# Performance work log

Measured on AMD Instinct MI355X. Metric: run time of the kernel, lower is better.

The kernel has to match this reference:

```python
import jax, jax.numpy as jnp
import numpy as np

H = 1024        # hidden_size
I = 2048        # intermediate_size
E = 8           # num_experts
K = 2           # num_experts_per_tok
AUX_COEF = 0.01
Z_COEF = 0.001


def setup_inputs() -> dict:
    key = jax.random.key(0)
    ks = jax.random.split(key, 8)
    s = 0.02
    return {
        "hidden_states": jax.random.normal(ks[0], (1, 2048, H), dtype=jnp.float32),
        "router_w": jax.random.normal(ks[1], (H, E), dtype=jnp.float32) * s,
        "eg": jax.random.normal(ks[2], (E, H, I), dtype=jnp.float32) * s,  # gate_proj per expert
        "eu": jax.random.normal(ks[3], (E, H, I), dtype=jnp.float32) * s,  # up_proj per expert
        "ed": jax.random.normal(ks[4], (E, I, H), dtype=jnp.float32) * s,  # down_proj per expert
        "sg": jax.random.normal(ks[5], (H, I), dtype=jnp.float32) * s,     # shared expert gate
        "su": jax.random.normal(ks[6], (H, I), dtype=jnp.float32) * s,     # shared expert up
        "sd": jax.random.normal(ks[7], (I, H), dtype=jnp.float32) * s,     # shared expert down
    }


def reference(hidden_states, router_w, eg, eu, ed, sg, su, sd):
    B, S, _ = hidden_states.shape
    x = hidden_states.reshape(-1, H)  # [T, H]

    # shared expert (num_shared_experts = 1)
    shared = (jax.nn.silu(x @ sg) * (x @ su)) @ sd  # [T, H]

    # router: linear -> softmax -> top-k, renormalize top-k probs
    logits = x @ router_w                      # [T, E]
    probs = jax.nn.softmax(logits, axis=-1)
    topw, topi = jax.lax.top_k(probs, K)       # [T, K]
    topw = topw / jnp.sum(topw, axis=-1, keepdims=True)

    # combine weights [T, E]: weight of expert e for token t (0 if not routed)
    combine = jnp.sum(jax.nn.one_hot(topi, E, dtype=x.dtype) * topw[..., None], axis=1)

    # dense expert compute (mathematically identical to masked gather/scatter loop)
    g = jnp.einsum('th,ehi->eti', x, eg)       # [E, T, I]
    u = jnp.einsum('th,ehi->eti', x, eu)
    h = jax.nn.silu(g) * u
    expert_out = jnp.einsum('eti,eih->eth', h, ed)  # [E, T, H]
    routed = jnp.einsum('eth,te->th', expert_out, combine)

    output = (shared + routed).reshape(B, S, H)

    # aux losses: Switch-style load balancing + router z-loss
    f = jnp.mean(jax.nn.one_hot(topi, E, dtype=x.dtype), axis=(0, 1))  # fraction dispatched
    p = jnp.mean(probs, axis=0)                                        # mean router prob
    lb_loss = AUX_COEF * E * jnp.sum(f * p)
    z_loss = Z_COEF * jnp.mean(jax.nn.logsumexp(logits, axis=-1) ** 2)
    aux_loss = lb_loss + z_loss
    return output, aux_loss
```

## Files before the change

kernel.cpp:

```cpp
#include <hip/hip_runtime.h>
#include <hip/hip_bf16.h>
#include <stdint.h>

#define T_ 2048
#define H_ 1024
#define I_ 2048
#define E_ 8
#define NE_ 9

typedef __attribute__((ext_vector_type(8))) short bf16x8;
typedef __attribute__((ext_vector_type(4))) float f32x4;

__device__ __forceinline__ unsigned short f2bf(float f) {
  unsigned int u; __builtin_memcpy(&u, &f, 4);
  u = (u + 0x7fffu + ((u >> 16) & 1u)) >> 16;
  return (unsigned short)u;
}
__device__ __forceinline__ void cvt2(float a, float b, unsigned short* dst) {
  __hip_bfloat162 h = __float22bfloat162_rn(float2{a, b});
  __builtin_memcpy(dst, &h, 4);
}
__device__ __forceinline__ void gll16(const void* g, void* l) {
  __builtin_amdgcn_global_load_lds((const __attribute__((address_space(1))) void*)g,
                                   (__attribute__((address_space(3))) void*)l, 16, 0, 0);
}

__global__ __launch_bounds__(256) void k_router(
    const float* __restrict__ x, const float* __restrict__ rw,
    int* __restrict__ topi, float* __restrict__ topw,
    float* __restrict__ probs, float* __restrict__ lse2,
    float* __restrict__ outz) {
  int tid = threadIdx.x;
  {
    float4 zf = {0.f, 0.f, 0.f, 0.f};
    float4* ob = (float4*)(outz + (size_t)blockIdx.x * 4096);
#pragma unroll
    for (int i = 0; i < 4; i++) ob[i * 256 + tid] = zf;
  }
  __shared__ float lrw[E_ * H_];
#pragma unroll
  for (int i = 0; i < 8; i++) {
    int idx = i * 256 + tid;
    float4 v = ((const float4*)rw)[idx];
    int f = idx * 4; int h = f >> 3; int e0 = f & 7;
    lrw[(e0 + 0) * H_ + h] = v.x;
    lrw[(e0 + 1) * H_ + h] = v.y;
    lrw[(e0 + 2) * H_ + h] = v.z;
    lrw[(e0 + 3) * H_ + h] = v.w;
  }
  __syncthreads();
  int w = tid >> 6, lane = tid & 63;
  int t = blockIdx.x * 4 + w;
  const float* xp = x + (size_t)t * H_ + lane;
  float xr[16];
#pragma unroll
  for (int j = 0; j < 16; j++) xr[j] = xp[j * 64];
  float acc[E_];
#pragma unroll
  for (int e = 0; e < E_; e++) acc[e] = 0.f;
#pragma unroll
  for (int j = 0; j < 16; j++) {
    float xf = xr[j];
    const float* wp = &lrw[j * 64 + lane];
#pragma unroll
    for (int e = 0; e < E_; e++) acc[e] += xf * wp[e * H_];
  }
#pragma unroll
  for (int off = 32; off >= 1; off >>= 1) {
#pragma unroll
    for (int e = 0; e < E_; e++) acc[e] += __shfl_xor(acc[e], off, 64);
  }
  if (lane == 0) {
    float m = acc[0];
#pragma unroll
    for (int e = 1; e < E_; e++) m = fmaxf(m, acc[e]);
    float p[E_], s = 0.f;
#pragma unroll
    for (int e = 0; e < E_; e++) { p[e] = expf(acc[e] - m); s += p[e]; }
    float inv = 1.f / s;
#pragma unroll
    for (int e = 0; e < E_; e++) p[e] *= inv;
    float lse = m + logf(s);
    lse2[t] = lse * lse;
    float4 p0 = {p[0], p[1], p[2], p[3]}, p1 = {p[4], p[5], p[6], p[7]};
    ((float4*)(probs + t * 8))[0] = p0;
    ((float4*)(probs + t * 8))[1] = p1;
    int i0 = 0;
#pragma unroll
    for (int e = 1; e < E_; e++) if (p[e] > p[i0]) i0 = e;
    int i1 = (i0 == 0) ? 1 : 0;
#pragma unroll
    for (int e = 0; e < E_; e++) if (e != i0 && e != i1 && p[e] > p[i1]) i1 = e;
    float w0 = p[i0], w1 = p[i1], wsum = w0 + w1;
    topi[t * 2] = i0; topi[t * 2 + 1] = i1;
    topw[t * 2] = w0 / wsum; topw[t * 2 + 1] = w1 / wsum;
  }
}

__global__ __launch_bounds__(256) void k_sched(
    const float* __restrict__ probs, const float* __restrict__ lse2,
    const int* __restrict__ topi, const float* __restrict__ topw,
    int* cnt, int* poffs, float* out_aux,
    int* __restrict__ tok, float* __restrict__ wgt) {
  __shared__ float sp[256][9];
  __shared__ int sc[256][8];
  __shared__ int sbase[NE_];
  __shared__ int scur[8];
  int tid = threadIdx.x;
  float ps[9] = {0.f, 0.f, 0.f, 0.f, 0.f, 0.f, 0.f, 0.f, 0.f};
  int c[8] = {0, 0, 0, 0, 0, 0, 0, 0};
  for (int t = tid; t < T_; t += 256) {
#pragma unroll
    for (int e = 0; e < E_; e++) ps[e] += probs[t * 8 + e];
    ps[8] += lse2[t];
    c[topi[t * 2]]++; c[topi[t * 2 + 1]]++;
  }
#pragma unroll
  for (int e = 0; e < 9; e++) sp[tid][e] = ps[e];
#pragma unroll
  for (int e = 0; e < 8; e++) sc[tid][e] = c[e];
  __syncthreads();
  for (int s = 128; s > 0; s >>= 1) {
    if (tid < s) {
#pragma unroll
      for (int e = 0; e < 9; e++) sp[tid][e] += sp[tid + s][e];
#pragma unroll
      for (int e = 0; e < 8; e++) sc[tid][e] += sc[tid + s][e];
    }
    __syncthreads();
  }
  if (tid == 0) {
#pragma unroll
    for (int e = 0; e < E_; e++) cnt[e] = sc[0][e];
    cnt[E_] = T_;
    int po = 0;
    for (int e = 0; e < NE_; e++) {
      poffs[e] = po; sbase[e] = po;
      int ce = (e < E_) ? sc[0][e] : T_;
      po += ((ce + 127) >> 7) << 7;
    }
    poffs[NE_] = po;
    float lb = 0.f;
#pragma unroll
    for (int e = 0; e < E_; e++)
      lb += ((float)sc[0][e] / 4096.f) * (sp[0][e] / 2048.f);
    out_aux[0] = 0.01f * 8.f * lb + 0.001f * (sp[0][8] / 2048.f);
  }
  if (tid < 8) scur[tid] = 0;
  __syncthreads();
  for (int t = tid; t < T_; t += 256) {
    int e0 = topi[t * 2], e1 = topi[t * 2 + 1];
    int p0 = atomicAdd(&scur[e0], 1);
    int p1 = atomicAdd(&scur[e1], 1);
    tok[sbase[e0] + p0] = t; wgt[sbase[e0] + p0] = topw[t * 2];
    tok[sbase[e1] + p1] = t; wgt[sbase[e1] + p1] = topw[t * 2 + 1];
    tok[sbase[E_] + t] = t; wgt[sbase[E_] + t] = 1.f;
  }
}

#define PACK_BLKS 27648
#define PREP_GRID 28800
__global__ __launch_bounds__(256) void k_prep(
    const float* __restrict__ eg, const float* __restrict__ eu, const float* __restrict__ ed,
    const float* __restrict__ sg, const float* __restrict__ su, const float* __restrict__ sd,
    unsigned short* __restrict__ wgp, unsigned short* __restrict__ wup,
    unsigned short* __restrict__ wdp,
    const float* __restrict__ x, const int* __restrict__ cnt,
    const int* __restrict__ poffs, const int* __restrict__ tok,
    unsigned short* __restrict__ apack) {
  __shared__ __align__(16) float lds[32 * 68];
  int bz = blockIdx.x;
  int t = threadIdx.x;
  if (bz < PACK_BLKS) {
    int mat = bz >> 10, tile = bz & 1023;
    int grp = mat / NE_, e = mat % NE_;
    int K, N, kt, nt;
    if (grp == 2) { K = I_; N = H_; kt = tile >> 4; nt = tile & 15; }
    else          { K = H_; N = I_; kt = tile >> 5; nt = tile & 31; }
    const float* src; unsigned short* dst;
    if (grp == 0)      { src = (e < E_) ? eg + (size_t)e * H_ * I_ : sg; dst = wgp + (size_t)e * H_ * I_; }
    else if (grp == 1) { src = (e < E_) ? eu + (size_t)e * H_ * I_ : su; dst = wup + (size_t)e * H_ * I_; }
    else               { src = (e < E_) ? ed + (size_t)e * I_ * H_ : sd; dst = wdp + (size_t)e * I_ * H_; }

    const float* srcbase = src + (size_t)(kt * 32) * N + nt * 64;
    int r0 = t >> 4, c0 = (t & 15) * 4;
    float4 v0 = *(const float4*)(srcbase + (size_t)r0 * N + c0);
    float4 v1 = *(const float4*)(srcbase + (size_t)(r0 + 16) * N + c0);
    *(float4*)&lds[r0 * 68 + c0] = v0;
    *(float4*)&lds[(r0 + 16) * 68 + c0] = v1;
    __syncthreads();

    int q = t >> 6, nn = t & 63;
    unsigned short o[8];
#pragma unroll
    for (int j = 0; j < 8; j += 2) {
      float a = lds[(q * 8 + j) * 68 + nn];
      float b = lds[(q * 8 + j + 1) * 68 + nn];
      cvt2(a, b, &o[j]);
    }
    size_t tile_off = ((size_t)nt * (K / 32) + kt) * 2048;
    *(bf16x8*)&dst[tile_off + q * 512 + nn * 8] = *(bf16x8*)o;
  } else {
    int id = bz - PACK_BLKS;
    int kc = id & 7, mt = (id >> 3) & 15, e = id >> 7;
    int cnt_e = cnt[e];
    if (mt * 128 >= cnt_e) return;
    int po = poffs[e];
    int rt = (po >> 7) + mt;
    int m = t & 127, qh = t >> 7;
    int atok = tok[po + min(mt * 128 + m, cnt_e - 1)];
    const float* arow = x + (size_t)atok * H_;
    size_t abase = (size_t)rt * 32 * 4096;
#pragma unroll
    for (int ki = 0; ki < 4; ki++) {
      int kt = kc * 4 + ki;
#pragma unroll
      for (int qo = 0; qo < 2; qo++) {
        int q = qh + qo * 2;
        const float* s = arow + kt * 32 + q * 8;
        float4 v0 = *(const float4*)s, v1 = *(const float4*)(s + 4);
        unsigned short t8[8];
        cvt2(v0.x, v0.y, t8); cvt2(v0.z, v0.w, t8 + 2);
        cvt2(v1.x, v1.y, t8 + 4); cvt2(v1.z, v1.w, t8 + 6);
        *(bf16x8*)&apack[abase + (size_t)kt * 4096 + q * 1024 + m * 8] = *(bf16x8*)t8;
      }
    }
  }
}

#define G1_GRID 1792
__global__ __launch_bounds__(256) void k_gemm1(
    const unsigned short* __restrict__ apack,
    const unsigned short* __restrict__ wgp, const unsigned short* __restrict__ wup,
    const int* __restrict__ cnt, const int* __restrict__ poffs,
    unsigned short* __restrict__ hbuf) {
  int lin = blockIdx.x;
  int s = (lin & 7) * (G1_GRID / 8) + (lin >> 3);
  int rt = s >> 5, nt = s & 31;
  int rtTotal = poffs[NE_] >> 7;
  if (rt >= rtTotal) return;
  int ro = rt << 7;
  int e = 0;
#pragma unroll
  for (int i = 1; i < NE_; i++) if (poffs[i] <= ro) e = i;
  int po = poffs[e];
  int cnt_e = cnt[e];
  int mt = (ro - po) >> 7;

  __shared__ __align__(16) unsigned short As[2][4096];
  __shared__ __align__(16) unsigned short BgS[2][2048];
  __shared__ __align__(16) unsigned short BuS[2][2048];

  int tid = threadIdx.x;
  int lane = tid & 63, w = tid >> 6;
  int quad = lane >> 4, l15 = lane & 15;
  int wm = w >> 1, wn = w & 1;

  const unsigned short* abase = apack + (size_t)rt * 32 * 4096;
  const unsigned short* bgb = wgp + (size_t)e * H_ * I_ + (size_t)nt * 32 * 2048;
  const unsigned short* bub = wup + (size_t)e * H_ * I_ + (size_t)nt * 32 * 2048;

  f32x4 zero = {0.f, 0.f, 0.f, 0.f};
  f32x4 accg[4][2], accu[4][2];
#pragma unroll
  for (int mi = 0; mi < 4; mi++)
#pragma unroll
    for (int ni = 0; ni < 2; ni++) { accg[mi][ni] = zero; accu[mi][ni] = zero; }

#define STAGE1(kt, b) do { \
    const unsigned short* asrc = abase + (size_t)(kt) * 4096 + w * 1024 + lane * 8; \
    gll16(asrc, &As[b][w * 1024]); \
    gll16(asrc + 512, &As[b][w * 1024 + 512]); \
    gll16(bgb + (size_t)(kt) * 2048 + w * 512 + lane * 8, &BgS[b][w * 512]); \
    gll16(bub + (size_t)(kt) * 2048 + w * 512 + lane * 8, &BuS[b][w * 512]); \
  } while (0)

  STAGE1(0, 0);
  __syncthreads();
  for (int kt = 0; kt < 32; kt++) {
    int cur = kt & 1;
    if (kt < 31) STAGE1(kt + 1, cur ^ 1);
    bf16x8 af[4];
#pragma unroll
    for (int mi = 0; mi < 4; mi++)
      af[mi] = *(const bf16x8*)&As[cur][quad * 1024 + (wm * 64 + mi * 16 + l15) * 8];
#pragma unroll
    for (int ni = 0; ni < 2; ni++) {
      bf16x8 bg = *(const bf16x8*)&BgS[cur][quad * 512 + (wn * 32 + ni * 16 + l15) * 8];
      bf16x8 bu = *(const bf16x8*)&BuS[cur][quad * 512 + (wn * 32 + ni * 16 + l15) * 8];
#pragma unroll
      for (int mi = 0; mi < 4; mi++) {
        accg[mi][ni] = __builtin_amdgcn_mfma_f32_16x16x32_bf16(af[mi], bg, accg[mi][ni], 0, 0, 0);
        accu[mi][ni] = __builtin_amdgcn_mfma_f32_16x16x32_bf16(af[mi], bu, accu[mi][ni], 0, 0, 0);
      }
    }
    __syncthreads();
  }
#undef STAGE1

  size_t hbase = (size_t)rt * 64 * 4096;
  int rem = cnt_e - mt * 128;
#pragma unroll
  for (int ni = 0; ni < 2; ni++) {
    int cc = nt * 64 + wn * 32 + ni * 16 + l15;
    size_t cb = hbase + (size_t)(cc >> 5) * 4096 + (size_t)((cc >> 3) & 3) * 1024 + (cc & 7);
#pragma unroll
    for (int mi = 0; mi < 4; mi++)
#pragma unroll
      for (int r = 0; r < 4; r++) {
        int row = wm * 64 + mi * 16 + quad * 4 + r;
        if (row < rem) {
          float g = accg[mi][ni][r], u = accu[mi][ni][r];
          float sv = g / (1.f + __expf(-g));
          hbuf[cb + (size_t)row * 8] = f2bf(sv * u);
        }
      }
  }
}

#define G2_GRID 896
__global__ __launch_bounds__(256) void k_gemm2(
    const unsigned short* __restrict__ hbuf, const unsigned short* __restrict__ wdp,
    const int* __restrict__ cnt, const int* __restrict__ poffs,
    const int* __restrict__ tok, const float* __restrict__ wgt,
    float* __restrict__ out) {
  int lin = blockIdx.x;
  int s = (lin & 7) * (G2_GRID / 8) + (lin >> 3);
  int rt = s >> 4;
  int r4 = s & 15;
  int nt = r4 >> 1, kh = r4 & 1;
  int rtTotal = poffs[NE_] >> 7;
  if (rt >= rtTotal) return;
  int ro = rt << 7;
  int e = 0;
#pragma unroll
  for (int i = 1; i < NE_; i++) if (poffs[i] <= ro) e = i;
  int po = poffs[e];
  int cnt_e = cnt[e];
  int mt = (ro - po) >> 7;

  __shared__ __align__(16) unsigned short As[2][4096];
  __shared__ __align__(16) unsigned short BdS[2][4096];

  int tid = threadIdx.x;
  int lane = tid & 63, w = tid >> 6;
  int quad = lane >> 4, l15 = lane & 15;
  int wm = w >> 1, wn = w & 1;

  const unsigned short* abase = hbuf + (size_t)rt * 64 * 4096;
  const unsigned short* bb0 = wdp + (size_t)e * I_ * H_ + ((size_t)(2 * nt) * 64) * 2048;
  const unsigned short* bb1 = wdp + (size_t)e * I_ * H_ + ((size_t)(2 * nt + 1) * 64) * 2048;

  f32x4 zero = {0.f, 0.f, 0.f, 0.f};
  f32x4 acc[4][4];
#pragma unroll
  for (int mi = 0; mi < 4; mi++)
#pragma unroll
    for (int ni = 0; ni < 4; ni++) acc[mi][ni] = zero;

#define STAGE2(kt, b) do { \
    const unsigned short* asrc = abase + (size_t)(kt) * 4096 + w * 1024 + lane * 8; \
    gll16(asrc, &As[b][w * 1024]); \
    gll16(asrc + 512, &As[b][w * 1024 + 512]); \
    gll16(bb0 + (size_t)(kt) * 2048 + w * 512 + lane * 8, &BdS[b][w * 512]); \
    gll16(bb1 + (size_t)(kt) * 2048 + w * 512 + lane * 8, &BdS[b][2048 + w * 512]); \
  } while (0)

  int k0 = kh * 32;
  STAGE2(k0, 0);
  __syncthreads();
  for (int kk = 0; kk < 32; kk++) {
    int cur = kk & 1;
    if (kk < 31) STAGE2(k0 + kk + 1, cur ^ 1);
    bf16x8 af[4];
#pragma unroll
    for (int mi = 0; mi < 4; mi++)
      af[mi] = *(const bf16x8*)&As[cur][quad * 1024 + (wm * 64 + mi * 16 + l15) * 8];
#pragma unroll
    for (int ni = 0; ni < 4; ni++) {
      bf16x8 bd = *(const bf16x8*)&BdS[cur][wn * 2048 + quad * 512 + (ni * 16 + l15) * 8];
#pragma unroll
      for (int mi = 0; mi < 4; mi++)
        acc[mi][ni] = __builtin_amdgcn_mfma_f32_16x16x32_bf16(af[mi], bd, acc[mi][ni], 0, 0, 0);
    }
    __syncthreads();
  }
#undef STAGE2

  int rem = cnt_e - mt * 128;
#pragma unroll
  for (int mi = 0; mi < 4; mi++)
#pragma unroll
    for (int r = 0; r < 4; r++) {
      int row = wm * 64 + mi * 16 + quad * 4 + r;
      if (row < rem) {
        int g = po + mt * 128 + row;
        int tt = tok[g];
        float wt = wgt[g];
#pragma unroll
        for (int ni = 0; ni < 4; ni++) {
          int col = nt * 128 + wn * 64 + ni * 16 + l15;
          atomicAdd(&out[(size_t)tt * H_ + col], wt * acc[mi][ni][r]);
        }
      }
    }
}

extern "C" void kernel_launch(void* const* d_in, const int* in_sizes, int n_in,
                              void* d_out, int out_size, void* d_ws, size_t ws_size,
                              hipStream_t stream) {
  const float* x  = (const float*)d_in[0];
  const float* rw = (const float*)d_in[1];
  const float* eg = (const float*)d_in[2];
  const float* eu = (const float*)d_in[3];
  const float* ed = (const float*)d_in[4];
  const float* sg = (const float*)d_in[5];
  const float* su = (const float*)d_in[6];
  const float* sd = (const float*)d_in[7];
  float* out = (float*)d_out;
  char* ws = (char*)d_ws;

  int*   cnt  = (int*)(ws + 64);
  int*   poffs= (int*)(ws + 128);
  int*   topi = (int*)(ws + 4096);
  float* topw = (float*)(ws + 4096 + 16384);
  int*   tok  = (int*)(ws + 36864);
  float* wgt  = (float*)(ws + 66560);
  unsigned short* apack = (unsigned short*)(ws + 131072);
  unsigned short* hbuf  = (unsigned short*)(ws + 131072 + 14811136);
  float* probs = (float*)(ws + 44302336);
  float* lse2  = (float*)(ws + 44367872);
  unsigned short* wgp   = (unsigned short*)(ws + 131072 + 14811136 + 29491200);
  unsigned short* wup   = (unsigned short*)((char*)wgp + (size_t)NE_ * H_ * I_ * 2);
  unsigned short* wdp   = (unsigned short*)((char*)wup + (size_t)NE_ * H_ * I_ * 2);

  k_router<<<512, 256, 0, stream>>>(x, rw, topi, topw, probs, lse2, out);
  k_sched<<<1, 256, 0, stream>>>(probs, lse2, topi, topw, cnt, poffs,
                                 out + (size_t)T_ * H_, tok, wgt);
  k_prep<<<PREP_GRID, 256, 0, stream>>>(eg, eu, ed, sg, su, sd, wgp, wup, wdp,
                                        x, cnt, poffs, tok, apack);
  k_gemm1<<<G1_GRID, 256, 0, stream>>>(apack, wgp, wup, cnt, poffs, hbuf);
  k_gemm2<<<G2_GRID, 256, 0, stream>>>(hbuf, wdp, cnt, poffs, tok, wgt, out);
}
```

Before: 426.4 us.

## Fuse router with weight packing and parallelize scheduling across experts

Merges the router and the fp32→bf16 weight packing into one front kernel, so the large weight conversion runs alongside routing instead of after it. Expert counts and probability sums are gathered with per-block atomics, which removes the probs/lse2 buffers, and the single-block scheduler is replaced by a per-expert prefix-scan kernel. Weight packing now uses bigger slabs with wider stores, and A-packing is split into its own kernel. This adds a memset and one extra launch, and the atomic float sums change reduction order.

```diff
diff --git a/kernel.cpp b/kernel.cpp
--- a/kernel.cpp
+++ b/kernel.cpp
@@ -25,205 +25,235 @@
                                    (__attribute__((address_space(3))) void*)l, 16, 0, 0);
 }
 
-__global__ __launch_bounds__(256) void k_router(
+#define RTR_BLKS 512
+#define PW01_BLKS 2304
+#define PW2_BLKS 2304
+#define FRONT_GRID (RTR_BLKS + PW01_BLKS + PW2_BLKS)
+__global__ __launch_bounds__(256) void k_front(
     const float* __restrict__ x, const float* __restrict__ rw,
     int* __restrict__ topi, float* __restrict__ topw,
-    float* __restrict__ probs, float* __restrict__ lse2,
-    float* __restrict__ outz) {
-  int tid = threadIdx.x;
-  {
-    float4 zf = {0.f, 0.f, 0.f, 0.f};
-    float4* ob = (float4*)(outz + (size_t)blockIdx.x * 4096);
-#pragma unroll
-    for (int i = 0; i < 4; i++) ob[i * 256 + tid] = zf;
-  }
-  __shared__ float lrw[E_ * H_];
-#pragma unroll
-  for (int i = 0; i < 8; i++) {
-    int idx = i * 256 + tid;
-    float4 v = ((const float4*)rw)[idx];
-    int f = idx * 4; int h = f >> 3; int e0 = f & 7;
-    lrw[(e0 + 0) * H_ + h] = v.x;
-    lrw[(e0 + 1) * H_ + h] = v.y;
-    lrw[(e0 + 2) * H_ + h] = v.z;
-    lrw[(e0 + 3) * H_ + h] = v.w;
-  }
-  __syncthreads();
-  int w = tid >> 6, lane = tid & 63;
-  int t = blockIdx.x * 4 + w;
-  const float* xp = x + (size_t)t * H_ + lane;
-  float xr[16];
-#pragma unroll
-  for (int j = 0; j < 16; j++) xr[j] = xp[j * 64];
-  float acc[E_];
-#pragma unroll
-  for (int e = 0; e < E_; e++) acc[e] = 0.f;
-#pragma unroll
-  for (int j = 0; j < 16; j++) {
-    float xf = xr[j];
-    const float* wp = &lrw[j * 64 + lane];
-#pragma unroll
-    for (int e = 0; e < E_; e++) acc[e] += xf * wp[e * H_];
-  }
-#pragma unroll
-  for (int off = 32; off >= 1; off >>= 1) {
-#pragma unroll
-    for (int e = 0; e < E_; e++) acc[e] += __shfl_xor(acc[e], off, 64);
-  }
-  if (lane == 0) {
-    float m = acc[0];
-#pragma unroll
-    for (int e = 1; e < E_; e++) m = fmaxf(m, acc[e]);
-    float p[E_], s = 0.f;
-#pragma unroll
-    for (int e = 0; e < E_; e++) { p[e] = expf(acc[e] - m); s += p[e]; }
-    float inv = 1.f / s;
-#pragma unroll
-    for (int e = 0; e < E_; e++) p[e] *= inv;
-    float lse = m + logf(s);
-    lse2[t] = lse * lse;
-    float4 p0 = {p[0], p[1], p[2], p[3]}, p1 = {p[4], p[5], p[6], p[7]};
-    ((float4*)(probs + t * 8))[0] = p0;
-    ((float4*)(probs + t * 8))[1] = p1;
-    int i0 = 0;
-#pragma unroll
-    for (int e = 1; e < E_; e++) if (p[e] > p[i0]) i0 = e;
-    int i1 = (i0 == 0) ? 1 : 0;
-#pragma unroll
-    for (int e = 0; e < E_; e++) if (e != i0 && e != i1 && p[e] > p[i1]) i1 = e;
-    float w0 = p[i0], w1 = p[i1], wsum = w0 + w1;
-    topi[t * 2] = i0; topi[t * 2 + 1] = i1;
-    topw[t * 2] = w0 / wsum; topw[t * 2 + 1] = w1 / wsum;
-  }
-}
-
-__global__ __launch_bounds__(256) void k_sched(
-    const float* __restrict__ probs, const float* __restrict__ lse2,
-    const int* __restrict__ topi, const float* __restrict__ topw,
-    int* cnt, int* poffs, float* out_aux,
-    int* __restrict__ tok, float* __restrict__ wgt) {
-  __shared__ float sp[256][9];
-  __shared__ int sc[256][8];
-  __shared__ int sbase[NE_];
-  __shared__ int scur[8];
-  int tid = threadIdx.x;
-  float ps[9] = {0.f, 0.f, 0.f, 0.f, 0.f, 0.f, 0.f, 0.f, 0.f};
-  int c[8] = {0, 0, 0, 0, 0, 0, 0, 0};
-  for (int t = tid; t < T_; t += 256) {
-#pragma unroll
-    for (int e = 0; e < E_; e++) ps[e] += probs[t * 8 + e];
-    ps[8] += lse2[t];
-    c[topi[t * 2]]++; c[topi[t * 2 + 1]]++;
-  }
-#pragma unroll
-  for (int e = 0; e < 9; e++) sp[tid][e] = ps[e];
-#pragma unroll
-  for (int e = 0; e < 8; e++) sc[tid][e] = c[e];
-  __syncthreads();
-  for (int s = 128; s > 0; s >>= 1) {
-    if (tid < s) {
-#pragma unroll
-      for (int e = 0; e < 9; e++) sp[tid][e] += sp[tid + s][e];
-#pragma unroll
-      for (int e = 0; e < 8; e++) sc[tid][e] += sc[tid + s][e];
-    }
-    __syncthreads();
-  }
-  if (tid == 0) {
-#pragma unroll
-    for (int e = 0; e < E_; e++) cnt[e] = sc[0][e];
-    cnt[E_] = T_;
-    int po = 0;
-    for (int e = 0; e < NE_; e++) {
-      poffs[e] = po; sbase[e] = po;
-      int ce = (e < E_) ? sc[0][e] : T_;
-      po += ((ce + 127) >> 7) << 7;
-    }
-    poffs[NE_] = po;
-    float lb = 0.f;
-#pragma unroll
-    for (int e = 0; e < E_; e++)
-      lb += ((float)sc[0][e] / 4096.f) * (sp[0][e] / 2048.f);
-    out_aux[0] = 0.01f * 8.f * lb + 0.001f * (sp[0][8] / 2048.f);
-  }
-  if (tid < 8) scur[tid] = 0;
-  __syncthreads();
-  for (int t = tid; t < T_; t += 256) {
-    int e0 = topi[t * 2], e1 = topi[t * 2 + 1];
-    int p0 = atomicAdd(&scur[e0], 1);
-    int p1 = atomicAdd(&scur[e1], 1);
-    tok[sbase[e0] + p0] = t; wgt[sbase[e0] + p0] = topw[t * 2];
-    tok[sbase[e1] + p1] = t; wgt[sbase[e1] + p1] = topw[t * 2 + 1];
-    tok[sbase[E_] + t] = t; wgt[sbase[E_] + t] = 1.f;
-  }
-}
-
-#define PACK_BLKS 27648
-#define PREP_GRID 28800
-__global__ __launch_bounds__(256) void k_prep(
+    int* __restrict__ cnt, float* __restrict__ psum,
+    float* __restrict__ outz,
     const float* __restrict__ eg, const float* __restrict__ eu, const float* __restrict__ ed,
     const float* __restrict__ sg, const float* __restrict__ su, const float* __restrict__ sd,
     unsigned short* __restrict__ wgp, unsigned short* __restrict__ wup,
-    unsigned short* __restrict__ wdp,
+    unsigned short* __restrict__ wdp) {
+  __shared__ float smem[8192];
+  __shared__ float sprob[4][9];
+  __shared__ int shist[8];
+  int tid = threadIdx.x;
+  int bz = blockIdx.x;
+
+  if (bz < RTR_BLKS) {
+    {
+      float4 zf = {0.f, 0.f, 0.f, 0.f};
+      float4* ob = (float4*)(outz + (size_t)bz * 4096);
+#pragma unroll
+      for (int i = 0; i < 4; i++) ob[i * 256 + tid] = zf;
+    }
+    if (tid < 8) shist[tid] = 0;
+#pragma unroll
+    for (int i = 0; i < 8; i++) {
+      int idx = i * 256 + tid;
+      float4 v = ((const float4*)rw)[idx];
+      int f = idx * 4; int h = f >> 3; int e0 = f & 7;
+      smem[(e0 + 0) * H_ + h] = v.x;
+      smem[(e0 + 1) * H_ + h] = v.y;
+      smem[(e0 + 2) * H_ + h] = v.z;
+      smem[(e0 + 3) * H_ + h] = v.w;
+    }
+    __syncthreads();
+    int w = tid >> 6, lane = tid & 63;
+    int t = bz * 4 + w;
+    const float* xp = x + (size_t)t * H_ + lane;
+    float xr[16];
+#pragma unroll
+    for (int j = 0; j < 16; j++) xr[j] = xp[j * 64];
+    float acc[E_];
+#pragma unroll
+    for (int e = 0; e < E_; e++) acc[e] = 0.f;
+#pragma unroll
+    for (int j = 0; j < 16; j++) {
+      float xf = xr[j];
+      const float* wp = &smem[j * 64 + lane];
+#pragma unroll
+      for (int e = 0; e < E_; e++) acc[e] += xf * wp[e * H_];
+    }
+#pragma unroll
+    for (int off = 32; off >= 1; off >>= 1) {
+#pragma unroll
+      for (int e = 0; e < E_; e++) acc[e] += __shfl_xor(acc[e], off, 64);
+    }
+    if (lane == 0) {
+      float m = acc[0];
+#pragma unroll
+      for (int e = 1; e < E_; e++) m = fmaxf(m, acc[e]);
+      float p[E_], s = 0.f;
+#pragma unroll
+      for (int e = 0; e < E_; e++) { p[e] = expf(acc[e] - m); s += p[e]; }
+      float inv = 1.f / s;
+#pragma unroll
+      for (int e = 0; e < E_; e++) p[e] *= inv;
+      float lse = m + logf(s);
+#pragma unroll
+      for (int e = 0; e < E_; e++) sprob[w][e] = p[e];
+      sprob[w][8] = lse * lse;
+      int i0 = 0;
+#pragma unroll
+      for (int e = 1; e < E_; e++) if (p[e] > p[i0]) i0 = e;
+      int i1 = (i0 == 0) ? 1 : 0;
+#pragma unroll
+      for (int e = 0; e < E_; e++) if (e != i0 && e != i1 && p[e] > p[i1]) i1 = e;
+      float w0 = p[i0], w1 = p[i1], wsum = w0 + w1;
+      topi[t * 2] = i0; topi[t * 2 + 1] = i1;
+      topw[t * 2] = w0 / wsum; topw[t * 2 + 1] = w1 / wsum;
+      atomicAdd(&shist[i0], 1);
+      atomicAdd(&shist[i1], 1);
+    }
+    __syncthreads();
+    if (tid < 8 && shist[tid]) atomicAdd(&cnt[tid], shist[tid]);
+    if (tid < 9)
+      atomicAdd(&psum[tid], sprob[0][tid] + sprob[1][tid] + sprob[2][tid] + sprob[3][tid]);
+    return;
+  }
+
+  int pb = bz - RTR_BLKS;
+  const float* src; unsigned short* dst;
+  int K, N, slab;
+  if (pb < PW01_BLKS) {
+    int mat = pb >> 7;
+    slab = pb & 127;
+    int grp = mat / NE_, e = mat % NE_;
+    K = H_; N = I_;
+    if (grp == 0) { src = (e < E_) ? eg + (size_t)e * H_ * I_ : sg; dst = wgp + (size_t)e * H_ * I_; }
+    else          { src = (e < E_) ? eu + (size_t)e * H_ * I_ : su; dst = wup + (size_t)e * H_ * I_; }
+  } else {
+    int pb2 = pb - PW01_BLKS;
+    int e = pb2 >> 8;
+    slab = pb2 & 255;
+    K = I_; N = H_;
+    src = (e < E_) ? ed + (size_t)e * I_ * H_ : sd;
+    dst = wdp + (size_t)e * I_ * H_;
+  }
+  int k0 = slab * 8;
+  int kt = k0 >> 5, q = (k0 >> 3) & 3;
+  int npass = N >> 10;
+  int l_nt = tid >> 4;
+  int nn0 = (tid & 15) * 4;
+
+  for (int p = 0; p < npass; ++p) {
+    const float* srcp = src + (size_t)k0 * N + p * 1024;
+#pragma unroll
+    for (int i = 0; i < 8; i++) {
+      float4 v = *(const float4*)(srcp + (size_t)i * N + 4 * tid);
+      *(float4*)&smem[i * 1024 + 4 * tid] = v;
+    }
+    __syncthreads();
+    unsigned short obuf[32];
+#pragma unroll
+    for (int jj = 0; jj < 4; jj++) {
+      float4 a = *(const float4*)&smem[(2 * jj) * 1024 + l_nt * 64 + nn0];
+      float4 b = *(const float4*)&smem[(2 * jj + 1) * 1024 + l_nt * 64 + nn0];
+      cvt2(a.x, b.x, &obuf[0 * 8 + 2 * jj]);
+      cvt2(a.y, b.y, &obuf[1 * 8 + 2 * jj]);
+      cvt2(a.z, b.z, &obuf[2 * 8 + 2 * jj]);
+      cvt2(a.w, b.w, &obuf[3 * 8 + 2 * jj]);
+    }
+    int nt = p * 16 + l_nt;
+    size_t base = ((size_t)nt * (K / 32) + kt) * 2048 + q * 512 + (size_t)nn0 * 8;
+#pragma unroll
+    for (int ci = 0; ci < 4; ci++)
+      *(bf16x8*)&dst[base + ci * 8] = *(bf16x8*)&obuf[ci * 8];
+    __syncthreads();
+  }
+}
+
+__global__ __launch_bounds__(256) void k_sched2(
+    const int* __restrict__ topi, const float* __restrict__ topw,
+    int* __restrict__ cnt, int* __restrict__ poffs, const float* __restrict__ psum,
+    float* __restrict__ out_aux,
+    int* __restrict__ tok, float* __restrict__ wgt) {
+  int tid = threadIdx.x;
+  int e = blockIdx.x;
+  int pol[NE_ + 1];
+  {
+    int po = 0;
+#pragma unroll
+    for (int i = 0; i < NE_; i++) {
+      pol[i] = po;
+      int ce = (i < E_) ? cnt[i] : T_;
+      po += ((ce + 127) >> 7) << 7;
+    }
+    pol[NE_] = po;
+  }
+  if (e == E_) {
+    int p8 = pol[E_];
+    for (int t = tid; t < T_; t += 256) { tok[p8 + t] = t; wgt[p8 + t] = 1.f; }
+    if (tid == 0) {
+#pragma unroll
+      for (int i = 0; i <= NE_; i++) poffs[i] = pol[i];
+      cnt[E_] = T_;
+      float lb = 0.f;
+#pragma unroll
+      for (int i = 0; i < E_; i++)
+        lb += ((float)cnt[i] / 4096.f) * (psum[i] / 2048.f);
+      out_aux[0] = 0.01f * 8.f * lb + 0.001f * (psum[8] / 2048.f);
+    }
+    return;
+  }
+  __shared__ int sc2[256];
+  int t0 = tid * 8;
+  int m = 0;
+  int e0v[8], e1v[8];
+#pragma unroll
+  for (int i = 0; i < 8; i++) {
+    e0v[i] = topi[(t0 + i) * 2];
+    e1v[i] = topi[(t0 + i) * 2 + 1];
+    m += (e0v[i] == e) + (e1v[i] == e);
+  }
+  sc2[tid] = m;
+  __syncthreads();
+  for (int s = 1; s < 256; s <<= 1) {
+    int v = (tid >= s) ? sc2[tid - s] : 0;
+    __syncthreads();
+    sc2[tid] += v;
+    __syncthreads();
+  }
+  int pos = pol[e] + sc2[tid] - m;
+#pragma unroll
+  for (int i = 0; i < 8; i++) {
+    int tk = t0 + i;
+    if (e0v[i] == e) { tok[pos] = tk; wgt[pos] = topw[tk * 2]; pos++; }
+    if (e1v[i] == e) { tok[pos] = tk; wgt[pos] = topw[tk * 2 + 1]; pos++; }
+  }
+}
+
+__global__ __launch_bounds__(256) void k_packA(
     const float* __restrict__ x, const int* __restrict__ cnt,
     const int* __restrict__ poffs, const int* __restrict__ tok,
     unsigned short* __restrict__ apack) {
-  __shared__ __align__(16) float lds[32 * 68];
-  int bz = blockIdx.x;
+  int kc = blockIdx.x, mt = blockIdx.y, e = blockIdx.z;
+  int cnt_e = cnt[e];
+  if (mt * 128 >= cnt_e) return;
+  int po = poffs[e];
+  int rt = (po >> 7) + mt;
   int t = threadIdx.x;
-  if (bz < PACK_BLKS) {
-    int mat = bz >> 10, tile = bz & 1023;
-    int grp = mat / NE_, e = mat % NE_;
-    int K, N, kt, nt;
-    if (grp == 2) { K = I_; N = H_; kt = tile >> 4; nt = tile & 15; }
-    else          { K = H_; N = I_; kt = tile >> 5; nt = tile & 31; }
-    const float* src; unsigned short* dst;
-    if (grp == 0)      { src = (e < E_) ? eg + (size_t)e * H_ * I_ : sg; dst = wgp + (size_t)e * H_ * I_; }
-    else if (grp == 1) { src = (e < E_) ? eu + (size_t)e * H_ * I_ : su; dst = wup + (size_t)e * H_ * I_; }
-    else               { src = (e < E_) ? ed + (size_t)e * I_ * H_ : sd; dst = wdp + (size_t)e * I_ * H_; }
-
-    const float* srcbase = src + (size_t)(kt * 32) * N + nt * 64;
-    int r0 = t >> 4, c0 = (t & 15) * 4;
-    float4 v0 = *(const float4*)(srcbase + (size_t)r0 * N + c0);
-    float4 v1 = *(const float4*)(srcbase + (size_t)(r0 + 16) * N + c0);
-    *(float4*)&lds[r0 * 68 + c0] = v0;
-    *(float4*)&lds[(r0 + 16) * 68 + c0] = v1;
-    __syncthreads();
-
-    int q = t >> 6, nn = t & 63;
-    unsigned short o[8];
-#pragma unroll
-    for (int j = 0; j < 8; j += 2) {
-      float a = lds[(q * 8 + j) * 68 + nn];
-      float b = lds[(q * 8 + j + 1) * 68 + nn];
-      cvt2(a, b, &o[j]);
-    }
-    size_t tile_off = ((size_t)nt * (K / 32) + kt) * 2048;
-    *(bf16x8*)&dst[tile_off + q * 512 + nn * 8] = *(bf16x8*)o;
-  } else {
-    int id = bz - PACK_BLKS;
-    int kc = id & 7, mt = (id >> 3) & 15, e = id >> 7;
-    int cnt_e = cnt[e];
-    if (mt * 128 >= cnt_e) return;
-    int po = poffs[e];
-    int rt = (po >> 7) + mt;
-    int m = t & 127, qh = t >> 7;
-    int atok = tok[po + min(mt * 128 + m, cnt_e - 1)];
-    const float* arow = x + (size_t)atok * H_;
-    size_t abase = (size_t)rt * 32 * 4096;
-#pragma unroll
-    for (int ki = 0; ki < 4; ki++) {
-      int kt = kc * 4 + ki;
-#pragma unroll
-      for (int qo = 0; qo < 2; qo++) {
-        int q = qh + qo * 2;
-        const float* s = arow + kt * 32 + q * 8;
-        float4 v0 = *(const float4*)s, v1 = *(const float4*)(s + 4);
-        unsigned short t8[8];
-        cvt2(v0.x, v0.y, t8); cvt2(v0.z, v0.w, t8 + 2);
-        cvt2(v1.x, v1.y, t8 + 4); cvt2(v1.z, v1.w, t8 + 6);
-        *(bf16x8*)&apack[abase + (size_t)kt * 4096 + q * 1024 + m * 8] = *(bf16x8*)t8;
-      }
+  int m = t & 127, qh = t >> 7;
+  int atok = tok[po + min(mt * 128 + m, cnt_e - 1)];
+  const float* arow = x + (size_t)atok * H_;
+  size_t abase = (size_t)rt * 32 * 4096;
+#pragma unroll
+  for (int ki = 0; ki < 4; ki++) {
+    int kt = kc * 4 + ki;
+#pragma unroll
+    for (int qo = 0; qo < 2; qo++) {
+      int q = qh + qo * 2;
+      const float* s = arow + kt * 32 + q * 8;
+      float4 v0 = *(const float4*)s, v1 = *(const float4*)(s + 4);
+      unsigned short t8[8];
+      cvt2(v0.x, v0.y, t8); cvt2(v0.z, v0.w, t8 + 2);
+      cvt2(v1.x, v1.y, t8 + 4); cvt2(v1.z, v1.w, t8 + 6);
+      *(bf16x8*)&apack[abase + (size_t)kt * 4096 + q * 1024 + m * 8] = *(bf16x8*)t8;
     }
   }
 }
@@ -422,23 +452,25 @@
 
   int*   cnt  = (int*)(ws + 64);
   int*   poffs= (int*)(ws + 128);
+  float* psum = (float*)(ws + 192);
   int*   topi = (int*)(ws + 4096);
   float* topw = (float*)(ws + 4096 + 16384);
   int*   tok  = (int*)(ws + 36864);
   float* wgt  = (float*)(ws + 66560);
   unsigned short* apack = (unsigned short*)(ws + 131072);
   unsigned short* hbuf  = (unsigned short*)(ws + 131072 + 14811136);
-  float* probs = (float*)(ws + 44302336);
-  float* lse2  = (float*)(ws + 44367872);
   unsigned short* wgp   = (unsigned short*)(ws + 131072 + 14811136 + 29491200);
   unsigned short* wup   = (unsigned short*)((char*)wgp + (size_t)NE_ * H_ * I_ * 2);
   unsigned short* wdp   = (unsigned short*)((char*)wup + (size_t)NE_ * H_ * I_ * 2);
 
-  k_router<<<512, 256, 0, stream>>>(x, rw, topi, topw, probs, lse2, out);
-  k_sched<<<1, 256, 0, stream>>>(probs, lse2, topi, topw, cnt, poffs,
-                                 out + (size_t)T_ * H_, tok, wgt);
-  k_prep<<<PREP_GRID, 256, 0, stream>>>(eg, eu, ed, sg, su, sd, wgp, wup, wdp,
-                                        x, cnt, poffs, tok, apack);
+  hipMemsetAsync(ws, 0, 256, stream);
+
+  k_front<<<FRONT_GRID, 256, 0, stream>>>(x, rw, topi, topw, cnt, psum, out,
+                                          eg, eu, ed, sg, su, sd, wgp, wup, wdp);
+  k_sched2<<<NE_, 256, 0, stream>>>(topi, topw, cnt, poffs, psum,
+                                    out + (size_t)T_ * H_, tok, wgt);
+  dim3 ga(8, 16, NE_);
+  k_packA<<<ga, 256, 0, stream>>>(x, cnt, poffs, tok, apack);
   k_gemm1<<<G1_GRID, 256, 0, stream>>>(apack, wgp, wup, cnt, poffs, hbuf);
   k_gemm2<<<G2_GRID, 256, 0, stream>>>(hbuf, wdp, cnt, poffs, tok, wgt, out);
 }
```

Measured after the change: 433.6 us. About the same (+1.7%).
